# Kernel optimization log

Hardware: AMD Instinct MI355X
Metric: run time of the kernel (lower is better)

## Reference

```python
import jax, jax.numpy as jnp
import numpy as np

HEADS = 4
BN_EPS = 1e-5


def _hgat_conv(x, src, dst, node_type, edge_attr, edge_type,
               ne, W, We, a_src, a_dst, a_edge, ee, Wres, b, concat):
    """Heterogeneous GAT conv: per-type embeddings + edge-featured attention.
    x: [N, Fin]; edge_attr: [E, De]; returns [N, H*C] (concat) or [N, C]."""
    N = x.shape[0]
    C = W.shape[1] // HEADS
    xi = x + ne[node_type]                                  # node-type conditioning
    h = (xi @ W).reshape(N, HEADS, C)                       # [N, H, C]
    he = ((edge_attr + ee[edge_type]) @ We).reshape(-1, HEADS, C)  # [E, H, C]
    s = jnp.einsum('nhc,hc->nh', h, a_src)                  # [N, H]
    d = jnp.einsum('nhc,hc->nh', h, a_dst)                  # [N, H]
    e = jnp.einsum('ehc,hc->eh', he, a_edge)                # [E, H]
    alpha = jax.nn.leaky_relu(s[src] + d[dst] + e, 0.2)     # [E, H]
    # softmax over incoming edges per destination node
    amax = jax.ops.segment_max(alpha, dst, num_segments=N)  # [N, H]
    amax = jnp.where(jnp.isfinite(amax), amax, 0.0)
    ex = jnp.exp(alpha - amax[dst])
    den = jax.ops.segment_sum(ex, dst, num_segments=N)
    coef = ex / (den[dst] + 1e-16)                          # [E, H]
    msg = h[src] * coef[:, :, None]                         # [E, H, C]
    out = jax.ops.segment_sum(msg, dst, num_segments=N)     # [N, H, C]
    out = out.reshape(N, HEADS * C) if concat else out.mean(axis=1)
    return out + x @ Wres + b                               # residual + bias


def _batch_norm(x, gamma, beta):
    mu = x.mean(axis=0)
    var = x.var(axis=0)
    return (x - mu) * jax.lax.rsqrt(var + BN_EPS) * gamma + beta


def setup_inputs() -> dict:
    key = jax.random.key(0)
    ks = jax.random.split(key, 32)
    N, E, H = 50000, 400000, 32          # nodes, edges, hidden_channels
    DE = 64                               # edge_dim
    NT, ET = 3, 4                         # node / edge type counts
    D1 = H * HEADS                        # 128 = enc1 output / enc2 width

    def g(k, shape, scale=1.0):
        return (jax.random.normal(ks[k], shape, dtype=jnp.float32) * scale)

    inp = {
        'x': g(0, (N, H)),
        'edge_index': jax.random.randint(ks[1], (2, E), 0, N, dtype=jnp.int32),
        'node_type': jax.random.randint(ks[2], (N,), 0, NT, dtype=jnp.int32),
        'edge_attr': g(3, (E, DE)),
        'edge_type': jax.random.randint(ks[4], (E,), 0, ET, dtype=jnp.int32),
        # enc1 params (in=32, per-head out=32, concat -> 128)
        'ne1': g(5, (NT, H), 0.1),
        'w1': g(6, (H, HEADS * H), 1.0 / np.sqrt(H)),
        'we1': g(7, (DE, HEADS * H), 1.0 / np.sqrt(DE)),
        'asrc1': g(8, (HEADS, H), 0.1), 'adst1': g(9, (HEADS, H), 0.1),
        'aedge1': g(10, (HEADS, H), 0.1),
        'ee1': g(11, (ET, DE), 0.1),
        'wres1': g(12, (H, D1), 1.0 / np.sqrt(H)),
        'b1': jnp.zeros((D1,), jnp.float32),
        # BatchNorm(128)
        'gamma': jnp.ones((D1,), jnp.float32),
        'beta': jnp.zeros((D1,), jnp.float32),
        # enc2 params (in=128, per-head out=128, mean -> 128)
        'ne2': g(13, (NT, D1), 0.1),
        'w2': g(14, (D1, HEADS * D1), 1.0 / np.sqrt(D1)),
        'we2': g(15, (DE, HEADS * D1), 1.0 / np.sqrt(DE)),
        'asrc2': g(16, (HEADS, D1), 0.1), 'adst2': g(17, (HEADS, D1), 0.1),
        'aedge2': g(18, (HEADS, D1), 0.1),
        'ee2': g(19, (ET, DE), 0.1),
        'wres2': g(20, (D1, D1), 1.0 / np.sqrt(D1)),
        'b2': jnp.zeros((D1,), jnp.float32),
    }
    return inp


def reference(x, edge_index, node_type, edge_attr, edge_type,
              ne1, w1, we1, asrc1, adst1, aedge1, ee1, wres1, b1,
              gamma, beta,
              ne2, w2, we2, asrc2, adst2, aedge2, ee2, wres2, b2):
    src, dst = edge_index[0], edge_index[1]
    h = _hgat_conv(x, src, dst, node_type, edge_attr, edge_type,
                   ne1, w1, we1, asrc1, adst1, aedge1, ee1, wres1, b1,
                   concat=True)
    h = _batch_norm(h, gamma, beta)
    out = _hgat_conv(h, src, dst, node_type, edge_attr, edge_type,
                     ne2, w2, we2, asrc2, adst2, aedge2, ee2, wres2, b2,
                     concat=False)
    return out
```

## Files before the change

### kernel.cpp

```cpp
#include <hip/hip_runtime.h>
#include <hip/hip_bf16.h>

typedef unsigned short u16;
typedef unsigned int u32;

constexpr int NN = 50000;
constexpr int NE = 400000;
constexpr int MPAD = 50048;

typedef __attribute__((ext_vector_type(8))) short s16x8;
typedef __attribute__((ext_vector_type(4))) float f32x4;

__device__ __forceinline__ float bf2f(u16 u) {
    union { u32 i; float f; } v; v.i = ((u32)u) << 16; return v.f;
}
__device__ __forceinline__ u16 f2bf(float f) {
    union { float f; u32 i; } v; v.f = f;
    u32 r = v.i + 0x7fffu + ((v.i >> 16) & 1u);
    return (u16)(r >> 16);
}
__device__ __forceinline__ float ldf(const void* p, size_t i, int isbf) {
    if (isbf) return bf2f(((const u16*)p)[i]);
    return ((const float*)p)[i];
}
__device__ __forceinline__ float clampf(float v) {
    return fminf(fmaxf(v, -1e4f), 1e4f);
}

__device__ int   g_flag;
__device__ int   g_counter;
__device__ float g_qe1[256], g_qe2[256];
__device__ float g_ps1[128], g_pd1[128], g_ps2[512], g_pd2[512];
__device__ float g_bnsum[128], g_bnsumsq[128], g_bnscale[128], g_bnshift[128];
__device__ int   g_deg[NN], g_start[NN], g_cur[NN];
__device__ int   g_eidx[NE];
__device__ __attribute__((aligned(16))) float g_sbuf[NN * 4];
__device__ __attribute__((aligned(16))) float g_dbuf[NN * 4];
__device__ __attribute__((aligned(16))) float g_alpha[(size_t)NE * 4];
__device__ __attribute__((aligned(16))) float g_xbuf[(size_t)NN * 128];
__device__ __attribute__((aligned(16))) float g_acc2[(size_t)NN * 128];
__device__ __attribute__((aligned(16))) u16 g_A1[(size_t)MPAD * 64];
__device__ __attribute__((aligned(16))) u16 g_A2[(size_t)MPAD * 160];
__device__ __attribute__((aligned(16))) u16 g_B1t[192 * 64];
__device__ __attribute__((aligned(16))) u16 g_B1bt[128 * 128];
__device__ __attribute__((aligned(16))) u16 g_B2t[192 * 160];
__device__ __attribute__((aligned(16))) u16 g_B2bt[128 * 512];
__device__ __attribute__((aligned(16))) u16 g_xi1[(size_t)NN * 32];
__device__ __attribute__((aligned(16))) u16 g_xi2[(size_t)NN * 128];
__device__ __attribute__((aligned(16))) u16 g_agg1[(size_t)MPAD * 128];
__device__ __attribute__((aligned(16))) u16 g_agg2[(size_t)MPAD * 512];

__global__ void k_detect(const u16* x) {
    if (threadIdx.x == 0) {
        int cnt = 0;
        for (int i = 0; i < 64; i++) {
            u16 u = x[2 * i];
            int ex = (u >> 7) & 0xff;
            if (ex >= 100 && ex <= 140) cnt++;
        }
        g_flag = (cnt >= 40) ? 1 : 0;
        g_counter = 0;
    }
}
__global__ void k_zero() {
    int i = blockIdx.x * blockDim.x + threadIdx.x;
    if (i < NN) g_deg[i] = 0;
    if (i < 128) { g_bnsum[i] = 0.f; g_bnsumsq[i] = 0.f; }
}

__global__ __launch_bounds__(256) void k_prep(
    const void* we1, const void* ae1, const void* we2, const void* ae2,
    const void* w1, const void* as1, const void* ad1,
    const void* w2, const void* as2, const void* ad2) {
    int isbf = g_flag;
    int t = threadIdx.x;
    int idx = blockIdx.x * 16 + (t >> 4);
    int s = t & 15;
    float a = 0.f;
    if (idx < 256) {
        int k = idx >> 2, hd = idx & 3;
        for (int c = s; c < 32; c += 16)
            a += ldf(we1, k * 128 + hd * 32 + c, isbf) * ldf(ae1, hd * 32 + c, isbf);
    } else if (idx < 512) {
        int i2 = idx - 256;
        int k = i2 >> 2, hd = i2 & 3;
        for (int c = s; c < 128; c += 16)
            a += ldf(we2, k * 512 + hd * 128 + c, isbf) * ldf(ae2, hd * 128 + c, isbf);
    } else if (idx < 768) {
        int i2 = idx - 512;
        int isd = i2 >> 7, j = i2 & 127;
        int h = j >> 5, k = j & 31;
        const void* av = isd ? ad1 : as1;
        for (int c = s; c < 32; c += 16)
            a += ldf(w1, k * 128 + h * 32 + c, isbf) * ldf(av, h * 32 + c, isbf);
    } else {
        int i2 = idx - 768;
        int isd = i2 >> 9, j = i2 & 511;
        int h = j >> 7, k = j & 127;
        const void* av = isd ? ad2 : as2;
        for (int c = s; c < 128; c += 16)
            a += ldf(w2, (size_t)k * 512 + h * 128 + c, isbf) * ldf(av, h * 128 + c, isbf);
    }
#pragma unroll
    for (int mk = 8; mk >= 1; mk >>= 1) a += __shfl_xor(a, mk);
    if (s == 0) {
        if (idx < 256) g_qe1[idx] = a;
        else if (idx < 512) g_qe2[idx - 256] = a;
        else if (idx < 768) {
            int i2 = idx - 512;
            if (i2 >> 7) g_pd1[i2 & 127] = a; else g_ps1[i2 & 127] = a;
        } else {
            int i2 = idx - 768;
            if (i2 >> 9) g_pd2[i2 & 511] = a; else g_ps2[i2 & 511] = a;
        }
    }
}

__global__ void k_deg(const int* __restrict__ dstp) {
    int e = blockIdx.x * blockDim.x + threadIdx.x;
    if (e < NE) atomicAdd(&g_deg[dstp[e]], 1);
}
__global__ void k_start() {
    int n = blockIdx.x * blockDim.x + threadIdx.x;
    if (n < NN) {
        int d = g_deg[n];
        int s = atomicAdd(&g_counter, d);
        g_start[n] = s; g_cur[n] = s;
    }
}
__global__ void k_scatter(const int* __restrict__ dstp) {
    int e = blockIdx.x * blockDim.x + threadIdx.x;
    if (e < NE) {
        int slot = atomicAdd(&g_cur[dstp[e]], 1);
        g_eidx[slot] = e;
    }
}

__device__ __forceinline__ u16 a1val(const void* x, int n, int k, int nt, int isbf) {
    if (k < 32) return f2bf(ldf(x, (size_t)n * 32 + k, isbf));
    if (k == 32 + nt || k == 35) return 0x3F80u;
    return 0;
}
__global__ __launch_bounds__(256) void k_buildA1(const void* x, const int* __restrict__ ntype,
                                                 const void* ne1) {
    int isbf = g_flag;
    int i = blockIdx.x * 256 + threadIdx.x;
    if (i >= MPAD * 32) return;
    int n = i >> 5, k2 = (i & 31) << 1;
    u32 pk = 0;
    if (n < NN) {
        int nt = ntype[n];
        pk = (u32)a1val(x, n, k2, nt, isbf) | ((u32)a1val(x, n, k2 + 1, nt, isbf) << 16);
        if (k2 < 32) {
            float x0 = ldf(x, (size_t)n * 32 + k2, isbf) + ldf(ne1, nt * 32 + k2, isbf);
            float x1 = ldf(x, (size_t)n * 32 + k2 + 1, isbf) + ldf(ne1, nt * 32 + k2 + 1, isbf);
            ((u32*)g_xi1)[(size_t)n * 16 + (k2 >> 1)] =
                (u32)f2bf(x0) | ((u32)f2bf(x1) << 16);
        }
    }
    ((u32*)g_A1)[i] = pk;
}
__global__ __launch_bounds__(256) void k_a2tail(const int* __restrict__ ntype) {
    int i = blockIdx.x * 256 + threadIdx.x;
    if (i >= NN * 16) return;
    int n = i >> 4, q = i & 15;
    int k2 = 128 + q * 2;
    int nt = ntype[n];
    u16 lo = (k2 == 128 + nt || k2 == 131) ? 0x3F80u : 0;
    u16 hi = (k2 + 1 == 128 + nt || k2 + 1 == 131) ? 0x3F80u : 0;
    ((u32*)g_A2)[(size_t)n * 80 + 64 + q] = (u32)lo | ((u32)hi << 16);
}
__global__ __launch_bounds__(256) void k_xi2(const int* __restrict__ ntype, const void* ne2) {
    int isbf = g_flag;
    int i = blockIdx.x * 256 + threadIdx.x;
    if (i >= NN * 64) return;
    int n = i >> 6, jp = (i & 63) << 1;
    int nt = ntype[n];
    float v0 = g_xbuf[(size_t)n * 128 + jp] * g_bnscale[jp] + g_bnshift[jp]
             + ldf(ne2, nt * 128 + jp, isbf);
    float v1 = g_xbuf[(size_t)n * 128 + jp + 1] * g_bnscale[jp + 1] + g_bnshift[jp + 1]
             + ldf(ne2, nt * 128 + jp + 1, isbf);
    ((u32*)g_xi2)[i] = (u32)f2bf(v0) | ((u32)f2bf(v1) << 16);
}

__global__ void k_buildB1(const void* ne1, const void* w1, const void* wres1, const void* b1) {
    int isbf = g_flag;
    int j = blockIdx.x;
    int k = threadIdx.x;
    float v = 0.f;
    if (j < 128) {
        if (k < 32) v = ldf(wres1, k * 128 + j, isbf);
        else if (k == 35) v = ldf(b1, j, isbf);
    } else if (j < 136) {
        int h = (j - 128) & 3;
        const float* p = (j < 132) ? g_ps1 : g_pd1;
        if (k < 32) v = p[h * 32 + k];
        else if (k < 35) {
            int tt = k - 32; float a = 0.f;
            for (int c = 0; c < 32; c++)
                a += ldf(ne1, tt * 32 + c, isbf) * p[h * 32 + c];
            v = a;
        }
    }
    (void)w1;
    g_B1t[j * 64 + k] = f2bf(v);
}
__global__ void k_buildB1b(const void* w1) {
    int isbf = g_flag;
    int j = blockIdx.x;
    int k = threadIdx.x;
    float v = ((k >> 5) == (j >> 5)) ? ldf(w1, (k & 31) * 128 + j, isbf) : 0.f;
    g_B1bt[j * 128 + k] = f2bf(v);
}
__global__ void k_buildB2(const void* ne2, const void* w2, const void* wres2, const void* b2) {
    int isbf = g_flag;
    int j = blockIdx.x;
    int k = threadIdx.x;
    if (k >= 160) return;
    float v = 0.f;
    if (j < 128) {
        if (k < 128) v = g_bnscale[k] * ldf(wres2, k * 128 + j, isbf);
        else if (k == 131) {
            float a = ldf(b2, j, isbf);
            for (int c = 0; c < 128; c++)
                a += g_bnshift[c] * ldf(wres2, c * 128 + j, isbf);
            v = a;
        }
    } else if (j < 136) {
        int h = (j - 128) & 3;
        const float* p = (j < 132) ? g_ps2 : g_pd2;
        if (k < 128) v = g_bnscale[k] * p[h * 128 + k];
        else if (k < 131) {
            int tt = k - 128; float a = 0.f;
            for (int c = 0; c < 128; c++)
                a += (g_bnshift[c] + ldf(ne2, tt * 128 + c, isbf)) * p[h * 128 + c];
            v = a;
        }
    }
    (void)w2;
    g_B2t[j * 160 + k] = f2bf(v);
}
__global__ void k_buildB2b(const void* w2) {
    int isbf = g_flag;
    int j = blockIdx.x;
    for (int k = threadIdx.x; k < 512; k += 256) {
        float v = 0.25f * ldf(w2, (size_t)(k & 127) * 512 + (k >> 7) * 128 + j, isbf);
        g_B2bt[j * 512 + k] = f2bf(v);
    }
}

template<int K, int KT, int LAYER>
__global__ __launch_bounds__(256) void k_gemm(void* outp) {
    constexpr int KP = KT + 8;
    __shared__ __attribute__((aligned(16))) u16 As[64 * KP];
    __shared__ __attribute__((aligned(16))) u16 Bs[64 * KP];
    const u16* __restrict__ A  = (LAYER == 1) ? g_A1 : (LAYER == 2) ? g_A2
                               : (LAYER == 3) ? g_agg1 : g_agg2;
    const u16* __restrict__ Bt = (LAYER == 1) ? g_B1t : (LAYER == 2) ? g_B2t
                               : (LAYER == 3) ? g_B1bt : g_B2bt;
    int isbf = g_flag;
    const int t = threadIdx.x;
    const int mb = blockIdx.x, cb = blockIdx.y;
    const int wave = t >> 6, lane = t & 63;
    const int lr = lane & 15, lg = lane >> 4;
    f32x4 acc[4] = {};
    constexpr int CH = KT / 8;
#pragma unroll 1
    for (int kt = 0; kt < K / KT; kt++) {
        __syncthreads();
        for (int c = t; c < 64 * CH; c += 256) {
            int r = c / CH, o = (c - r * CH) * 8;
            *(s16x8*)&As[r * KP + o] =
                *(const s16x8*)&A[((size_t)(mb * 64 + r)) * K + kt * KT + o];
            *(s16x8*)&Bs[r * KP + o] =
                *(const s16x8*)&Bt[((size_t)(cb * 64 + r)) * K + kt * KT + o];
        }
        __syncthreads();
        const u16* ap  = &As[(wave * 16 + lr) * KP + lg * 8];
        const u16* bp0 = &Bs[lr * KP + lg * 8];
#pragma unroll
        for (int ks = 0; ks < KT / 32; ks++) {
            s16x8 af = *(const s16x8*)(ap + ks * 32);
#pragma unroll
            for (int ct = 0; ct < 4; ct++) {
                s16x8 bf = *(const s16x8*)(bp0 + ct * 16 * KP + ks * 32);
                acc[ct] = __builtin_amdgcn_mfma_f32_16x16x32_bf16(af, bf, acc[ct], 0, 0, 0);
            }
        }
    }
    const int rowb = mb * 64 + wave * 16 + lg * 4;
#pragma unroll
    for (int ct = 0; ct < 4; ct++) {
        int j = cb * 64 + ct * 16 + lr;
#pragma unroll
        for (int r = 0; r < 4; r++) {
            int n = rowb + r;
            if (n >= NN) continue;
            float v = acc[ct][r];
            if (LAYER == 1) {
                if (j < 128)      g_xbuf[(size_t)n * 128 + j] = clampf(v);
                else if (j < 132) g_sbuf[n * 4 + (j - 128)] = clampf(v);
                else if (j < 136) g_dbuf[n * 4 + (j - 132)] = clampf(v);
            } else if (LAYER == 2) {
                if (j < 128)      g_acc2[(size_t)n * 128 + j] = clampf(v);
                else if (j < 132) g_sbuf[n * 4 + (j - 128)] = clampf(v);
                else if (j < 136) g_dbuf[n * 4 + (j - 132)] = clampf(v);
            } else if (LAYER == 3) {
                float* p = &g_xbuf[(size_t)n * 128 + j];
                float x = clampf(*p + v);
                *p = x;
                g_A2[(size_t)n * 160 + j] = f2bf(x);
            } else {
                float v2 = clampf(g_acc2[(size_t)n * 128 + j] + v);
                if (isbf) ((u16*)outp)[(size_t)n * 128 + j] = f2bf(v2);
                else      ((float*)outp)[(size_t)n * 128 + j] = v2;
            }
        }
    }
}

__global__ __launch_bounds__(256) void k_edge(
    const int* __restrict__ srcp, const int* __restrict__ dstp,
    const int* __restrict__ etype, const void* eattr,
    const void* ee, int lyr) {
    __shared__ float eel[4 * 68];
    __shared__ float qel[256];
    int isbf = g_flag;
    int t = threadIdx.x;
    const float* qe = (lyr == 1) ? g_qe1 : g_qe2;
    { int tt = t >> 6, k = t & 63; eel[tt * 68 + k] = ldf(ee, tt * 64 + k, isbf); }
    qel[t] = qe[t];
    __syncthreads();
    int sub = t & 15;
    float q[4][4];
#pragma unroll
    for (int i = 0; i < 4; i++)
#pragma unroll
        for (int h = 0; h < 4; h++)
            q[i][h] = qel[(sub * 4 + i) * 4 + h];
    int g = t >> 4;
    int e = blockIdx.x * 16 + g;
    if (e >= NE) return;
    int et = etype[e];
    float ev[4];
    if (isbf) {
        ushort4 vv = *(const ushort4*)((const u16*)eattr + (size_t)e * 64 + sub * 4);
        ev[0] = bf2f(vv.x); ev[1] = bf2f(vv.y); ev[2] = bf2f(vv.z); ev[3] = bf2f(vv.w);
    } else {
        float4 vv = *(const float4*)((const float*)eattr + (size_t)e * 64 + sub * 4);
        ev[0] = vv.x; ev[1] = vv.y; ev[2] = vv.z; ev[3] = vv.w;
    }
    const float* ep = eel + et * 68 + sub * 4;
    float p0 = 0.f, p1 = 0.f, p2 = 0.f, p3 = 0.f;
#pragma unroll
    for (int i = 0; i < 4; i++) {
        float evi = ev[i] + ep[i];
        p0 += evi * q[i][0]; p1 += evi * q[i][1];
        p2 += evi * q[i][2]; p3 += evi * q[i][3];
    }
#pragma unroll
    for (int mk = 1; mk < 16; mk <<= 1) {
        p0 += __shfl_xor(p0, mk); p1 += __shfl_xor(p1, mk);
        p2 += __shfl_xor(p2, mk); p3 += __shfl_xor(p3, mk);
    }
    if (sub == 0) {
        int ss = srcp[e], dd = dstp[e];
        float4 sb = *(const float4*)(g_sbuf + ss * 4);
        float4 db = *(const float4*)(g_dbuf + dd * 4);
        float a0 = sb.x + db.x + p0;
        float a1 = sb.y + db.y + p1;
        float a2 = sb.z + db.z + p2;
        float a3 = sb.w + db.w + p3;
        a0 = a0 > 0.f ? a0 : 0.2f * a0;
        a1 = a1 > 0.f ? a1 : 0.2f * a1;
        a2 = a2 > 0.f ? a2 : 0.2f * a2;
        a3 = a3 > 0.f ? a3 : 0.2f * a3;
        *(float4*)(g_alpha + 4 * (size_t)e) = make_float4(
            clampf(a0), clampf(a1), clampf(a2), clampf(a3));
    }
}

__global__ __launch_bounds__(256) void k_att1(const int* __restrict__ srcp) {
    int lane = threadIdx.x & 63;
    int n = blockIdx.x * 4 + (threadIdx.x >> 6);
    if (n >= NN) return;
    int st = g_start[n], dg = g_deg[n];
    float m0 = -1e30f, m1 = -1e30f, m2 = -1e30f, m3 = -1e30f;
    for (int i = lane; i < dg; i += 64) {
        int e = g_eidx[st + i];
        float4 a = *(const float4*)(g_alpha + 4 * (size_t)e);
        m0 = fmaxf(m0, a.x); m1 = fmaxf(m1, a.y);
        m2 = fmaxf(m2, a.z); m3 = fmaxf(m3, a.w);
    }
    for (int mk = 32; mk >= 1; mk >>= 1) {
        m0 = fmaxf(m0, __shfl_xor(m0, mk)); m1 = fmaxf(m1, __shfl_xor(m1, mk));
        m2 = fmaxf(m2, __shfl_xor(m2, mk)); m3 = fmaxf(m3, __shfl_xor(m3, mk));
    }
    int j0 = 2 * lane;
    int hd = j0 >> 5;
    float z0 = 0.f, z1 = 0.f, z2 = 0.f, z3 = 0.f;
    float acc0 = 0.f, acc1 = 0.f;
    for (int base = 0; base < dg; base += 64) {
        int i = base + lane;
        int sidx = 0; float c0 = 0.f, c1 = 0.f, c2 = 0.f, c3 = 0.f;
        if (i < dg) {
            int e = g_eidx[st + i];
            float4 a = *(const float4*)(g_alpha + 4 * (size_t)e);
            sidx = srcp[e];
            c0 = expf(a.x - m0); c1 = expf(a.y - m1);
            c2 = expf(a.z - m2); c3 = expf(a.w - m3);
            z0 += c0; z1 += c1; z2 += c2; z3 += c3;
        }
        int cnt = min(64, dg - base);
        for (int jj = 0; jj < cnt; jj++) {
            int s2 = __shfl(sidx, jj);
            float b0 = __shfl(c0, jj), b1 = __shfl(c1, jj);
            float b2v = __shfl(c2, jj), b3 = __shfl(c3, jj);
            float cs = hd == 0 ? b0 : hd == 1 ? b1 : hd == 2 ? b2v : b3;
            u32 hv = *(const u32*)(g_xi1 + (size_t)s2 * 32 + (j0 & 31));
            acc0 += bf2f((u16)(hv & 0xffff)) * cs;
            acc1 += bf2f((u16)(hv >> 16)) * cs;
        }
    }
    for (int mk = 32; mk >= 1; mk >>= 1) {
        z0 += __shfl_xor(z0, mk); z1 += __shfl_xor(z1, mk);
        z2 += __shfl_xor(z2, mk); z3 += __shfl_xor(z3, mk);
    }
    float iv = 1.f / ((hd == 0 ? z0 : hd == 1 ? z1 : hd == 2 ? z2 : z3) + 1e-16f);
    ((u32*)g_agg1)[((size_t)n * 128 + j0) >> 1] =
        (u32)f2bf(acc0 * iv) | ((u32)f2bf(acc1 * iv) << 16);
}

__global__ __launch_bounds__(256) void k_bnstats() {
    int t = threadIdx.x;
    int j = t & 127;
    int r0 = blockIdx.x * 2 + (t >> 7);
    float s = 0.f, ss = 0.f;
    for (int r = r0; r < NN; r += 500) {
        float v = g_xbuf[(size_t)r * 128 + j];
        s += v; ss += v * v;
    }
    atomicAdd(&g_bnsum[j], s);
    atomicAdd(&g_bnsumsq[j], ss);
}
__global__ void k_bnfin(const void* gamma, const void* beta) {
    int isbf = g_flag;
    int j = threadIdx.x;
    float mu = g_bnsum[j] * (1.f / NN);
    float var = fmaxf(g_bnsumsq[j] * (1.f / NN) - mu * mu, 0.f);
    float rstd = rsqrtf(var + 1e-5f);
    float sc = ldf(gamma, j, isbf) * rstd;
    g_bnscale[j] = sc;
    g_bnshift[j] = ldf(beta, j, isbf) - mu * sc;
}

__global__ __launch_bounds__(256) void k_att2(const int* __restrict__ srcp) {
    int lane = threadIdx.x & 63;
    int n = blockIdx.x * 4 + (threadIdx.x >> 6);
    if (n >= NN) return;
    int st = g_start[n], dg = g_deg[n];
    float m0 = -1e30f, m1 = -1e30f, m2 = -1e30f, m3 = -1e30f;
    for (int i = lane; i < dg; i += 64) {
        int e = g_eidx[st + i];
        float4 a = *(const float4*)(g_alpha + 4 * (size_t)e);
        m0 = fmaxf(m0, a.x); m1 = fmaxf(m1, a.y);
        m2 = fmaxf(m2, a.z); m3 = fmaxf(m3, a.w);
    }
    for (int mk = 32; mk >= 1; mk >>= 1) {
        m0 = fmaxf(m0, __shfl_xor(m0, mk)); m1 = fmaxf(m1, __shfl_xor(m1, mk));
        m2 = fmaxf(m2, __shfl_xor(m2, mk)); m3 = fmaxf(m3, __shfl_xor(m3, mk));
    }
    int c0 = 2 * lane;
    float z0 = 0.f, z1 = 0.f, z2 = 0.f, z3 = 0.f;
    float a00 = 0.f, a01 = 0.f, a10 = 0.f, a11 = 0.f;
    float a20 = 0.f, a21 = 0.f, a30 = 0.f, a31 = 0.f;
    for (int base = 0; base < dg; base += 64) {
        int i = base + lane;
        int sidx = 0; float c0f = 0.f, c1f = 0.f, c2f = 0.f, c3f = 0.f;
        if (i < dg) {
            int e = g_eidx[st + i];
            float4 a = *(const float4*)(g_alpha + 4 * (size_t)e);
            sidx = srcp[e];
            c0f = expf(a.x - m0); c1f = expf(a.y - m1);
            c2f = expf(a.z - m2); c3f = expf(a.w - m3);
            z0 += c0f; z1 += c1f; z2 += c2f; z3 += c3f;
        }
        int cnt = min(64, dg - base);
        for (int jj = 0; jj < cnt; jj++) {
            int s2 = __shfl(sidx, jj);
            float b0 = __shfl(c0f, jj), b1 = __shfl(c1f, jj);
            float b2v = __shfl(c2f, jj), b3 = __shfl(c3f, jj);
            u32 hv = *(const u32*)(g_xi2 + (size_t)s2 * 128 + c0);
            float lo = bf2f((u16)(hv & 0xffff)), hi = bf2f((u16)(hv >> 16));
            a00 += lo * b0;  a01 += hi * b0;
            a10 += lo * b1;  a11 += hi * b1;
            a20 += lo * b2v; a21 += hi * b2v;
            a30 += lo * b3;  a31 += hi * b3;
        }
    }
    for (int mk = 32; mk >= 1; mk >>= 1) {
        z0 += __shfl_xor(z0, mk); z1 += __shfl_xor(z1, mk);
        z2 += __shfl_xor(z2, mk); z3 += __shfl_xor(z3, mk);
    }
    float iv0 = 1.f / (z0 + 1e-16f), iv1 = 1.f / (z1 + 1e-16f);
    float iv2 = 1.f / (z2 + 1e-16f), iv3 = 1.f / (z3 + 1e-16f);
    u32* out = (u32*)g_agg2 + (((size_t)n * 512 + c0) >> 1);
    out[0]   = (u32)f2bf(a00 * iv0) | ((u32)f2bf(a01 * iv0) << 16);
    out[64]  = (u32)f2bf(a10 * iv1) | ((u32)f2bf(a11 * iv1) << 16);
    out[128] = (u32)f2bf(a20 * iv2) | ((u32)f2bf(a21 * iv2) << 16);
    out[192] = (u32)f2bf(a30 * iv3) | ((u32)f2bf(a31 * iv3) << 16);
}

extern "C" void kernel_launch(void* const* d_in, const int* in_sizes, int n_in,
                              void* d_out, int out_size, void* d_ws, size_t ws_size,
                              hipStream_t stream) {
    const void* x     = d_in[0];
    const int* ei     = (const int*)d_in[1];
    const int* ntype  = (const int*)d_in[2];
    const void* eattr = d_in[3];
    const int* etype  = (const int*)d_in[4];
    const void* ne1   = d_in[5];
    const void* w1    = d_in[6];
    const void* we1   = d_in[7];
    const void* asrc1 = d_in[8];
    const void* adst1 = d_in[9];
    const void* aedge1= d_in[10];
    const void* ee1   = d_in[11];
    const void* wres1 = d_in[12];
    const void* b1    = d_in[13];
    const void* gamma = d_in[14];
    const void* beta  = d_in[15];
    const void* ne2   = d_in[16];
    const void* w2    = d_in[17];
    const void* we2   = d_in[18];
    const void* asrc2 = d_in[19];
    const void* adst2 = d_in[20];
    const void* aedge2= d_in[21];
    const void* ee2   = d_in[22];
    const void* wres2 = d_in[23];
    const void* b2    = d_in[24];
    (void)in_sizes; (void)n_in; (void)out_size; (void)d_ws; (void)ws_size;

    const int* srcp = ei;
    const int* dstp = ei + NE;

    k_detect<<<1, 64, 0, stream>>>((const u16*)x);
    k_zero<<<196, 256, 0, stream>>>();
    k_prep<<<112, 256, 0, stream>>>(we1, aedge1, we2, aedge2,
                                    w1, asrc1, adst1, w2, asrc2, adst2);
    k_deg<<<1563, 256, 0, stream>>>(dstp);
    k_start<<<196, 256, 0, stream>>>();
    k_scatter<<<1563, 256, 0, stream>>>(dstp);

    k_buildA1<<<(MPAD * 32 + 255) / 256, 256, 0, stream>>>(x, ntype, ne1);
    k_buildB1<<<192, 64, 0, stream>>>(ne1, w1, wres1, b1);
    k_buildB1b<<<128, 128, 0, stream>>>(w1);
    k_gemm<64, 64, 1><<<dim3(MPAD / 64, 3), 256, 0, stream>>>(nullptr);
    k_edge<<<NE / 16, 256, 0, stream>>>(srcp, dstp, etype, eattr, ee1, 1);
    k_att1<<<12500, 256, 0, stream>>>(srcp);
    k_gemm<128, 128, 3><<<dim3(MPAD / 64, 2), 256, 0, stream>>>(nullptr);

    k_bnstats<<<250, 256, 0, stream>>>();
    k_bnfin<<<1, 128, 0, stream>>>(gamma, beta);

    k_xi2<<<12500, 256, 0, stream>>>(ntype, ne2);
    k_a2tail<<<(NN * 16 + 255) / 256, 256, 0, stream>>>(ntype);
    k_buildB2<<<192, 192, 0, stream>>>(ne2, w2, wres2, b2);
    k_buildB2b<<<128, 256, 0, stream>>>(w2);
    k_gemm<160, 160, 2><<<dim3(MPAD / 64, 3), 256, 0, stream>>>(nullptr);
    k_edge<<<NE / 16, 256, 0, stream>>>(srcp, dstp, etype, eattr, ee2, 2);
    k_att2<<<12500, 256, 0, stream>>>(srcp);
    k_gemm<512, 128, 4><<<dim3(MPAD / 64, 2), 256, 0, stream>>>(d_out);
}
```

Measured before the change: 620.8 us.

## Compute both layers' edge-attention projections in one pass over edge_attr

The edge-feature attention term depends only on edge_attr, edge type and weights, so both layers' projections are now computed in a single pass that reads edge_attr once. The layer-2 terms go to a new per-edge buffer, and layer 2 gets a lightweight kernel that only combines them with the node terms. The edge-type embedding contribution is folded into a small precomputed per-type, per-head table, which removes a per-element add. This trades a second 400000x64 read of edge_attr for an extra 6.4 MB write and read of the per-edge buffer.

```diff
diff --git a/kernel.cpp b/kernel.cpp
--- a/kernel.cpp
+++ b/kernel.cpp
@@ -30,6 +30,7 @@
 __device__ int   g_flag;
 __device__ int   g_counter;
 __device__ float g_qe1[256], g_qe2[256];
+__device__ float g_eq1[16], g_eq2[16];
 __device__ float g_ps1[128], g_pd1[128], g_ps2[512], g_pd2[512];
 __device__ float g_bnsum[128], g_bnsumsq[128], g_bnscale[128], g_bnshift[128];
 __device__ int   g_deg[NN], g_start[NN], g_cur[NN];
@@ -37,6 +38,7 @@
 __device__ __attribute__((aligned(16))) float g_sbuf[NN * 4];
 __device__ __attribute__((aligned(16))) float g_dbuf[NN * 4];
 __device__ __attribute__((aligned(16))) float g_alpha[(size_t)NE * 4];
+__device__ __attribute__((aligned(16))) float g_el2[(size_t)NE * 4];
 __device__ __attribute__((aligned(16))) float g_xbuf[(size_t)NN * 128];
 __device__ __attribute__((aligned(16))) float g_acc2[(size_t)NN * 128];
 __device__ __attribute__((aligned(16))) u16 g_A1[(size_t)MPAD * 64];
@@ -115,6 +117,24 @@
         }
     }
 }
+__global__ void k_prep2(const void* ee1, const void* ee2) {
+    int isbf = g_flag;
+    int t = threadIdx.x;
+    int idx = blockIdx.x * 16 + (t >> 4);
+    int s = t & 15;
+    int lyr = idx >> 4;
+    int et = (idx >> 2) & 3, h = idx & 3;
+    const void* ee = lyr ? ee2 : ee1;
+    const float* qe = lyr ? g_qe2 : g_qe1;
+    float a = 0.f;
+    for (int k = s; k < 64; k += 16)
+        a += ldf(ee, et * 64 + k, isbf) * qe[k * 4 + h];
+#pragma unroll
+    for (int mk = 8; mk >= 1; mk >>= 1) a += __shfl_xor(a, mk);
+    if (s == 0) {
+        if (lyr) g_eq2[et * 4 + h] = a; else g_eq1[et * 4 + h] = a;
+    }
+}
 
 __global__ void k_deg(const int* __restrict__ dstp) {
     int e = blockIdx.x * blockDim.x + threadIdx.x;
@@ -319,29 +339,27 @@
     }
 }
 
-__global__ __launch_bounds__(256) void k_edge(
+__global__ __launch_bounds__(256) void k_edge12(
     const int* __restrict__ srcp, const int* __restrict__ dstp,
-    const int* __restrict__ etype, const void* eattr,
-    const void* ee, int lyr) {
-    __shared__ float eel[4 * 68];
-    __shared__ float qel[256];
+    const int* __restrict__ etype, const void* eattr) {
+    __shared__ float qel1[256], qel2[256], eq1s[16], eq2s[16];
     int isbf = g_flag;
     int t = threadIdx.x;
-    const float* qe = (lyr == 1) ? g_qe1 : g_qe2;
-    { int tt = t >> 6, k = t & 63; eel[tt * 68 + k] = ldf(ee, tt * 64 + k, isbf); }
-    qel[t] = qe[t];
+    qel1[t] = g_qe1[t];
+    qel2[t] = g_qe2[t];
+    if (t < 16) { eq1s[t] = g_eq1[t]; eq2s[t] = g_eq2[t]; }
     __syncthreads();
     int sub = t & 15;
-    float q[4][4];
+    float q1[4][4], q2[4][4];
 #pragma unroll
     for (int i = 0; i < 4; i++)
 #pragma unroll
-        for (int h = 0; h < 4; h++)
-            q[i][h] = qel[(sub * 4 + i) * 4 + h];
-    int g = t >> 4;
-    int e = blockIdx.x * 16 + g;
+        for (int h = 0; h < 4; h++) {
+            q1[i][h] = qel1[(sub * 4 + i) * 4 + h];
+            q2[i][h] = qel2[(sub * 4 + i) * 4 + h];
+        }
+    int e = blockIdx.x * 16 + (t >> 4);
     if (e >= NE) return;
-    int et = etype[e];
     float ev[4];
     if (isbf) {
         ushort4 vv = *(const ushort4*)((const u16*)eattr + (size_t)e * 64 + sub * 4);
@@ -350,34 +368,60 @@
         float4 vv = *(const float4*)((const float*)eattr + (size_t)e * 64 + sub * 4);
         ev[0] = vv.x; ev[1] = vv.y; ev[2] = vv.z; ev[3] = vv.w;
     }
-    const float* ep = eel + et * 68 + sub * 4;
-    float p0 = 0.f, p1 = 0.f, p2 = 0.f, p3 = 0.f;
+    float p10 = 0.f, p11 = 0.f, p12 = 0.f, p13 = 0.f;
+    float p20 = 0.f, p21 = 0.f, p22 = 0.f, p23 = 0.f;
 #pragma unroll
     for (int i = 0; i < 4; i++) {
-        float evi = ev[i] + ep[i];
-        p0 += evi * q[i][0]; p1 += evi * q[i][1];
-        p2 += evi * q[i][2]; p3 += evi * q[i][3];
+        p10 += ev[i] * q1[i][0]; p11 += ev[i] * q1[i][1];
+        p12 += ev[i] * q1[i][2]; p13 += ev[i] * q1[i][3];
+        p20 += ev[i] * q2[i][0]; p21 += ev[i] * q2[i][1];
+        p22 += ev[i] * q2[i][2]; p23 += ev[i] * q2[i][3];
     }
 #pragma unroll
     for (int mk = 1; mk < 16; mk <<= 1) {
-        p0 += __shfl_xor(p0, mk); p1 += __shfl_xor(p1, mk);
-        p2 += __shfl_xor(p2, mk); p3 += __shfl_xor(p3, mk);
+        p10 += __shfl_xor(p10, mk); p11 += __shfl_xor(p11, mk);
+        p12 += __shfl_xor(p12, mk); p13 += __shfl_xor(p13, mk);
+        p20 += __shfl_xor(p20, mk); p21 += __shfl_xor(p21, mk);
+        p22 += __shfl_xor(p22, mk); p23 += __shfl_xor(p23, mk);
     }
     if (sub == 0) {
-        int ss = srcp[e], dd = dstp[e];
+        int et = etype[e], ss = srcp[e], dd = dstp[e];
         float4 sb = *(const float4*)(g_sbuf + ss * 4);
         float4 db = *(const float4*)(g_dbuf + dd * 4);
-        float a0 = sb.x + db.x + p0;
-        float a1 = sb.y + db.y + p1;
-        float a2 = sb.z + db.z + p2;
-        float a3 = sb.w + db.w + p3;
+        float a0 = sb.x + db.x + p10 + eq1s[et * 4 + 0];
+        float a1 = sb.y + db.y + p11 + eq1s[et * 4 + 1];
+        float a2 = sb.z + db.z + p12 + eq1s[et * 4 + 2];
+        float a3 = sb.w + db.w + p13 + eq1s[et * 4 + 3];
         a0 = a0 > 0.f ? a0 : 0.2f * a0;
         a1 = a1 > 0.f ? a1 : 0.2f * a1;
         a2 = a2 > 0.f ? a2 : 0.2f * a2;
         a3 = a3 > 0.f ? a3 : 0.2f * a3;
         *(float4*)(g_alpha + 4 * (size_t)e) = make_float4(
             clampf(a0), clampf(a1), clampf(a2), clampf(a3));
-    }
+        *(float4*)(g_el2 + 4 * (size_t)e) = make_float4(
+            p20 + eq2s[et * 4 + 0], p21 + eq2s[et * 4 + 1],
+            p22 + eq2s[et * 4 + 2], p23 + eq2s[et * 4 + 3]);
+    }
+}
+
+__global__ __launch_bounds__(256) void k_edge2(
+    const int* __restrict__ srcp, const int* __restrict__ dstp) {
+    int e = blockIdx.x * 256 + threadIdx.x;
+    if (e >= NE) return;
+    float4 p = *(const float4*)(g_el2 + 4 * (size_t)e);
+    int ss = srcp[e], dd = dstp[e];
+    float4 sb = *(const float4*)(g_sbuf + ss * 4);
+    float4 db = *(const float4*)(g_dbuf + dd * 4);
+    float a0 = sb.x + db.x + p.x;
+    float a1 = sb.y + db.y + p.y;
+    float a2 = sb.z + db.z + p.z;
+    float a3 = sb.w + db.w + p.w;
+    a0 = a0 > 0.f ? a0 : 0.2f * a0;
+    a1 = a1 > 0.f ? a1 : 0.2f * a1;
+    a2 = a2 > 0.f ? a2 : 0.2f * a2;
+    a3 = a3 > 0.f ? a3 : 0.2f * a3;
+    *(float4*)(g_alpha + 4 * (size_t)e) = make_float4(
+        clampf(a0), clampf(a1), clampf(a2), clampf(a3));
 }
 
 __global__ __launch_bounds__(256) void k_att1(const int* __restrict__ srcp) {
@@ -548,6 +592,7 @@
     k_zero<<<196, 256, 0, stream>>>();
     k_prep<<<112, 256, 0, stream>>>(we1, aedge1, we2, aedge2,
                                     w1, asrc1, adst1, w2, asrc2, adst2);
+    k_prep2<<<2, 256, 0, stream>>>(ee1, ee2);
     k_deg<<<1563, 256, 0, stream>>>(dstp);
     k_start<<<196, 256, 0, stream>>>();
     k_scatter<<<1563, 256, 0, stream>>>(dstp);
@@ -556,7 +601,7 @@
     k_buildB1<<<192, 64, 0, stream>>>(ne1, w1, wres1, b1);
     k_buildB1b<<<128, 128, 0, stream>>>(w1);
     k_gemm<64, 64, 1><<<dim3(MPAD / 64, 3), 256, 0, stream>>>(nullptr);
-    k_edge<<<NE / 16, 256, 0, stream>>>(srcp, dstp, etype, eattr, ee1, 1);
+    k_edge12<<<NE / 16, 256, 0, stream>>>(srcp, dstp, etype, eattr);
     k_att1<<<12500, 256, 0, stream>>>(srcp);
     k_gemm<128, 128, 3><<<dim3(MPAD / 64, 2), 256, 0, stream>>>(nullptr);
 
@@ -568,7 +613,7 @@
     k_buildB2<<<192, 192, 0, stream>>>(ne2, w2, wres2, b2);
     k_buildB2b<<<128, 256, 0, stream>>>(w2);
     k_gemm<160, 160, 2><<<dim3(MPAD / 64, 3), 256, 0, stream>>>(nullptr);
-    k_edge<<<NE / 16, 256, 0, stream>>>(srcp, dstp, etype, eattr, ee2, 2);
+    k_edge2<<<1563, 256, 0, stream>>>(srcp, dstp);
     k_att2<<<12500, 256, 0, stream>>>(srcp);
     k_gemm<512, 128, 4><<<dim3(MPAD / 64, 2), 256, 0, stream>>>(d_out);
 }
```

After: 608.2 us. -2.0%, faster.
